# Optimization experiments

Measured on AMD Instinct MI355X. Metric: run time of the kernel, lower is better.

The kernel has to match this reference:

```python
import jax, jax.numpy as jnp
import numpy as np

B, N, L, D = 128, 1024, 512, 64


def setup_inputs() -> dict:
    key = jax.random.key(0)
    k1, k2 = jax.random.split(key)
    text_outputs = jax.random.normal(k1, (B, N, D), dtype=jnp.float32)
    image_outputs = jax.random.normal(k2, (B, L, D), dtype=jnp.float32)
    rng = np.random.RandomState(0)
    ntok = rng.randint(N // 4, N + 1, size=B)
    nreg = rng.randint(L // 4, L + 1, size=B)
    text_mask = (np.arange(N)[None, :] < ntok[:, None]).astype(np.float32)
    image_mask = (np.arange(L)[None, :] < nreg[:, None]).astype(np.float32)
    # impostor indices (torch code samples these with np.random inside forward;
    # here they are fixed constants for determinism), guaranteed != own index
    I_imp = rng.randint(0, B, size=B)
    S_imp = rng.randint(0, B, size=B)
    ar = np.arange(B)
    I_imp = np.where(I_imp == ar, (I_imp + 1) % B, I_imp).astype(np.int32)
    S_imp = np.where(S_imp == ar, (S_imp + 1) % B, S_imp).astype(np.int32)
    return {
        "text_outputs": text_outputs,
        "image_outputs": image_outputs,
        "text_mask": jnp.asarray(text_mask),
        "image_mask": jnp.asarray(image_mask),
        "I_imp_idx": jnp.asarray(I_imp),
        "S_imp_idx": jnp.asarray(S_imp),
    }


def _mean_max_sim(T, I, tmask, imask):
    # T: (N, D) tokens, I: (L, D) regions; masks select the ragged valid prefix.
    M = jnp.einsum('nd,ld->nl', T, I)                       # matchmap (N, L)
    neg = jnp.finfo(M.dtype).min
    mx = jnp.max(jnp.where(imask[None, :] > 0, M, neg), axis=1)  # max over regions
    return jnp.sum(mx * tmask) / jnp.sum(tmask)             # mean over valid tokens


def reference(text_outputs, image_outputs, text_mask, image_mask, I_imp_idx, S_imp_idx, margin=1.0):
    sim = jax.vmap(_mean_max_sim)
    anchor = sim(text_outputs, image_outputs, text_mask, image_mask)            # (B,)
    Simpsim = sim(text_outputs[S_imp_idx], image_outputs, text_mask[S_imp_idx], image_mask)
    Iimpsim = sim(text_outputs, image_outputs[I_imp_idx], text_mask, image_mask[I_imp_idx])
    # scalar per-sample hinge: term added only when margin+imp-anchor > 0 == relu
    per_sample = jax.nn.relu(margin + Iimpsim - anchor) + jax.nn.relu(margin + Simpsim - anchor)
    loss = jnp.sum(per_sample) / text_outputs.shape[0]
    return loss[None]  # torch returns shape (1,)
```

## Files before the change

kernel.cpp:

```cpp
#include <hip/hip_runtime.h>

#define B 128
#define N 1024
#define L 512
#define D 64

typedef float f32x4 __attribute__((ext_vector_type(4)));
typedef short bf16x8 __attribute__((ext_vector_type(8)));

__device__ inline unsigned int pack_bf16(float lo, float hi) {
    unsigned int a = __float_as_uint(lo), b = __float_as_uint(hi);
    a = (a + 0x7fffu + ((a >> 16) & 1u)) >> 16;
    b = (b + 0x7fffu + ((b >> 16) & 1u)) & 0xffff0000u;
    return a | b;
}

__global__ __launch_bounds__(256, 2) void sim_kernel(
        const float* __restrict__ T, const float* __restrict__ I,
        const float* __restrict__ tmask, const float* __restrict__ imask,
        const int* __restrict__ Iimp, const int* __restrict__ Simp,
        float* __restrict__ sims) {
    int blk = blockIdx.x;
    int s = blk >> 7;
    int b = blk & (B - 1);
    int Tb = b, Ib = b;
    if (s == 1) Tb = Simp[b];
    else if (s == 2) Ib = Iimp[b];

    int tid = threadIdx.x;
    int w = tid >> 6;
    int lane = tid & 63;
    int q = lane >> 4;
    int c = lane & 15;

    __shared__ unsigned short ldsI[L * D];
    float* redf = (float*)ldsI;

    float ts = 0.f, is = 0.f;
    {
        const float* tm = tmask + (size_t)Tb * N;
        for (int i = tid; i < N; i += 256) ts += tm[i];
        const float* im = imask + (size_t)Ib * L;
        for (int i = tid; i < L; i += 256) is += im[i];
    }
    for (int off = 32; off > 0; off >>= 1) {
        ts += __shfl_down(ts, off);
        is += __shfl_down(is, off);
    }
    if (lane == 0) { redf[w] = ts; redf[4 + w] = is; }
    __syncthreads();
    int ntok = (int)(redf[0] + redf[1] + redf[2] + redf[3] + 0.5f);
    int nreg = (int)(redf[4] + redf[5] + redf[6] + redf[7] + 0.5f);
    __syncthreads();

    int full_rt = nreg >> 4;
    int rem = nreg & 15;
    int nrt = full_rt + (rem ? 1 : 0);
    int nchunk = nrt * 128;
    const float* Ibase = I + (size_t)Ib * L * D;
    for (int ci = tid; ci < nchunk; ci += 256) {
        int rt = ci >> 7;
        int h = (ci >> 6) & 1;
        int ln = ci & 63;
        int r = rt * 16 + (ln & 15);
        int dbase = h * 32 + (ln >> 4) * 8;
        uint4 outv = make_uint4(0u, 0u, 0u, 0u);
        if (r < nreg) {
            const float4* p = (const float4*)(Ibase + (size_t)r * D + dbase);
            float4 f0 = p[0], f1 = p[1];
            outv.x = pack_bf16(f0.x, f0.y);
            outv.y = pack_bf16(f0.z, f0.w);
            outv.z = pack_bf16(f1.x, f1.y);
            outv.w = pack_bf16(f1.z, f1.w);
        }
        *(uint4*)((char*)ldsI + (size_t)ci * 16) = outv;
    }
    __syncthreads();

    const char* ldsB = (const char*)ldsI + (size_t)lane * 16;
    float bsum = 0.f;
    for (int tok0 = 0; tok0 < ntok; tok0 += 256) {
        int wt0 = tok0 + w * 64;
        bf16x8 afrag[4][2];
#pragma unroll
        for (int tt = 0; tt < 4; ++tt) {
            const float* trow = T + ((size_t)Tb * N + wt0 + tt * 16 + c) * D;
#pragma unroll
            for (int h = 0; h < 2; ++h) {
                const float4* p = (const float4*)(trow + h * 32 + q * 8);
                float4 f0 = p[0], f1 = p[1];
                unsigned int u[4];
                u[0] = pack_bf16(f0.x, f0.y);
                u[1] = pack_bf16(f0.z, f0.w);
                u[2] = pack_bf16(f1.x, f1.y);
                u[3] = pack_bf16(f1.z, f1.w);
                afrag[tt][h] = *(bf16x8*)u;
            }
        }

        float mx[4][4];
#pragma unroll
        for (int tt = 0; tt < 4; ++tt)
#pragma unroll
            for (int i = 0; i < 4; ++i) mx[tt][i] = -3.0e38f;

#pragma unroll 1
        for (int rt = 0; rt < full_rt; ++rt) {
            bf16x8 b0 = *(const bf16x8*)(ldsB + (size_t)(rt * 2 + 0) * 1024);
            bf16x8 b1 = *(const bf16x8*)(ldsB + (size_t)(rt * 2 + 1) * 1024);
#pragma unroll
            for (int tt = 0; tt < 4; ++tt) {
                f32x4 acc = {0.f, 0.f, 0.f, 0.f};
                acc = __builtin_amdgcn_mfma_f32_16x16x32_bf16(afrag[tt][0], b0, acc, 0, 0, 0);
                acc = __builtin_amdgcn_mfma_f32_16x16x32_bf16(afrag[tt][1], b1, acc, 0, 0, 0);
#pragma unroll
                for (int i = 0; i < 4; ++i) mx[tt][i] = fmaxf(mx[tt][i], acc[i]);
            }
        }
        if (rem) {
            bf16x8 b0 = *(const bf16x8*)(ldsB + (size_t)(full_rt * 2 + 0) * 1024);
            bf16x8 b1 = *(const bf16x8*)(ldsB + (size_t)(full_rt * 2 + 1) * 1024);
            bool valid = c < rem;
#pragma unroll
            for (int tt = 0; tt < 4; ++tt) {
                f32x4 acc = {0.f, 0.f, 0.f, 0.f};
                acc = __builtin_amdgcn_mfma_f32_16x16x32_bf16(afrag[tt][0], b0, acc, 0, 0, 0);
                acc = __builtin_amdgcn_mfma_f32_16x16x32_bf16(afrag[tt][1], b1, acc, 0, 0, 0);
                if (valid) {
#pragma unroll
                    for (int i = 0; i < 4; ++i) mx[tt][i] = fmaxf(mx[tt][i], acc[i]);
                }
            }
        }

#pragma unroll
        for (int m = 1; m < 16; m <<= 1) {
#pragma unroll
            for (int tt = 0; tt < 4; ++tt)
#pragma unroll
                for (int i = 0; i < 4; ++i)
                    mx[tt][i] = fmaxf(mx[tt][i], __shfl_xor(mx[tt][i], m));
        }
        if (c == 0) {
#pragma unroll
            for (int tt = 0; tt < 4; ++tt)
#pragma unroll
                for (int i = 0; i < 4; ++i) {
                    int row = wt0 + tt * 16 + q * 4 + i;
                    if (row < ntok) bsum += mx[tt][i];
                }
        }
    }

    for (int off = 32; off > 0; off >>= 1) bsum += __shfl_down(bsum, off);
    __syncthreads();
    if (lane == 0) redf[8 + w] = bsum;
    __syncthreads();
    if (tid == 0)
        sims[s * B + b] = (redf[8] + redf[9] + redf[10] + redf[11]) / (float)ntok;
}

__global__ void loss_kernel(const float* __restrict__ sims,
                            float* __restrict__ out) {
    int tid = threadIdx.x;
    float anc = sims[tid];
    float simp = sims[B + tid];
    float iimp = sims[2 * B + tid];
    float per = fmaxf(1.f + iimp - anc, 0.f) + fmaxf(1.f + simp - anc, 0.f);
    for (int off = 32; off > 0; off >>= 1) per += __shfl_down(per, off);
    __shared__ float w2[2];
    if ((tid & 63) == 0) w2[tid >> 6] = per;
    __syncthreads();
    if (tid == 0) out[0] = (w2[0] + w2[1]) / (float)B;
}

extern "C" void kernel_launch(void* const* d_in, const int* in_sizes, int n_in,
                              void* d_out, int out_size, void* d_ws, size_t ws_size,
                              hipStream_t stream) {
    const float* T     = (const float*)d_in[0];
    const float* I     = (const float*)d_in[1];
    const float* tmask = (const float*)d_in[2];
    const float* imask = (const float*)d_in[3];
    const int*   Iimp  = (const int*)d_in[4];
    const int*   Simp  = (const int*)d_in[5];
    float* sims = (float*)d_ws;

    sim_kernel<<<3 * B, 256, 0, stream>>>(T, I, tmask, imask, Iimp, Simp, sims);
    loss_kernel<<<1, 128, 0, stream>>>(sims, (float*)d_out);
}
```

Measured before the change: 138.4 us.

## Split token range across four blocks per pair and stream image tiles from global

```diff
diff --git a/kernel.cpp b/kernel.cpp
--- a/kernel.cpp
+++ b/kernel.cpp
@@ -1,4 +1,5 @@
 #include <hip/hip_runtime.h>
+#include <hip/hip_bf16.h>
 
 #define B 128
 #define N 1024
@@ -8,21 +9,25 @@
 typedef float f32x4 __attribute__((ext_vector_type(4)));
 typedef short bf16x8 __attribute__((ext_vector_type(8)));
 
-__device__ inline unsigned int pack_bf16(float lo, float hi) {
-    unsigned int a = __float_as_uint(lo), b = __float_as_uint(hi);
-    a = (a + 0x7fffu + ((a >> 16) & 1u)) >> 16;
-    b = (b + 0x7fffu + ((b >> 16) & 1u)) & 0xffff0000u;
-    return a | b;
+__device__ inline bf16x8 cvt8(float4 f0, float4 f1) {
+    union { __hip_bfloat162 h2[4]; bf16x8 v; } u;
+    u.h2[0] = __float22bfloat162_rn(make_float2(f0.x, f0.y));
+    u.h2[1] = __float22bfloat162_rn(make_float2(f0.z, f0.w));
+    u.h2[2] = __float22bfloat162_rn(make_float2(f1.x, f1.y));
+    u.h2[3] = __float22bfloat162_rn(make_float2(f1.z, f1.w));
+    return u.v;
 }
 
-__global__ __launch_bounds__(256, 2) void sim_kernel(
+__global__ __launch_bounds__(256, 4) void sim_kernel(
         const float* __restrict__ T, const float* __restrict__ I,
         const float* __restrict__ tmask, const float* __restrict__ imask,
         const int* __restrict__ Iimp, const int* __restrict__ Simp,
-        float* __restrict__ sims) {
+        float* __restrict__ partials) {
     int blk = blockIdx.x;
-    int s = blk >> 7;
-    int b = blk & (B - 1);
+    int chunk = blk & 3;
+    int bs = blk >> 2;
+    int b = bs & (B - 1);
+    int s = bs >> 7;
     int Tb = b, Ib = b;
     if (s == 1) Tb = Simp[b];
     else if (s == 2) Ib = Iimp[b];
@@ -33,8 +38,7 @@
     int q = lane >> 4;
     int c = lane & 15;
 
-    __shared__ unsigned short ldsI[L * D];
-    float* redf = (float*)ldsI;
+    __shared__ float red[12];
 
     float ts = 0.f, is = 0.f;
     {
@@ -47,131 +51,120 @@
         ts += __shfl_down(ts, off);
         is += __shfl_down(is, off);
     }
-    if (lane == 0) { redf[w] = ts; redf[4 + w] = is; }
+    if (lane == 0) { red[w] = ts; red[4 + w] = is; }
     __syncthreads();
-    int ntok = (int)(redf[0] + redf[1] + redf[2] + redf[3] + 0.5f);
-    int nreg = (int)(redf[4] + redf[5] + redf[6] + redf[7] + 0.5f);
-    __syncthreads();
+    int ntok = (int)(red[0] + red[1] + red[2] + red[3] + 0.5f);
+    int nreg = (int)(red[4] + red[5] + red[6] + red[7] + 0.5f);
+
+    int tok0 = chunk * 256;
+    if (tok0 >= ntok) {
+        if (tid == 0) partials[blk] = 0.f;
+        return;
+    }
+
+    int wt0 = tok0 + w * 64;
+    bf16x8 afrag[4][2];
+#pragma unroll
+    for (int tt = 0; tt < 4; ++tt) {
+        const float* trow = T + ((size_t)Tb * N + wt0 + tt * 16 + c) * D;
+#pragma unroll
+        for (int h = 0; h < 2; ++h) {
+            const float4* p = (const float4*)(trow + h * 32 + q * 8);
+            afrag[tt][h] = cvt8(p[0], p[1]);
+        }
+    }
+
+    float mx[4][4];
+#pragma unroll
+    for (int tt = 0; tt < 4; ++tt)
+#pragma unroll
+        for (int i = 0; i < 4; ++i) mx[tt][i] = -3.0e38f;
+
+    const float* Ip = I + (size_t)Ib * L * D + (size_t)c * D + q * 8;
 
     int full_rt = nreg >> 4;
     int rem = nreg & 15;
-    int nrt = full_rt + (rem ? 1 : 0);
-    int nchunk = nrt * 128;
-    const float* Ibase = I + (size_t)Ib * L * D;
-    for (int ci = tid; ci < nchunk; ci += 256) {
-        int rt = ci >> 7;
-        int h = (ci >> 6) & 1;
-        int ln = ci & 63;
-        int r = rt * 16 + (ln & 15);
-        int dbase = h * 32 + (ln >> 4) * 8;
-        uint4 outv = make_uint4(0u, 0u, 0u, 0u);
-        if (r < nreg) {
-            const float4* p = (const float4*)(Ibase + (size_t)r * D + dbase);
-            float4 f0 = p[0], f1 = p[1];
-            outv.x = pack_bf16(f0.x, f0.y);
-            outv.y = pack_bf16(f0.z, f0.w);
-            outv.z = pack_bf16(f1.x, f1.y);
-            outv.w = pack_bf16(f1.z, f1.w);
-        }
-        *(uint4*)((char*)ldsI + (size_t)ci * 16) = outv;
-    }
-    __syncthreads();
 
-    const char* ldsB = (const char*)ldsI + (size_t)lane * 16;
-    float bsum = 0.f;
-    for (int tok0 = 0; tok0 < ntok; tok0 += 256) {
-        int wt0 = tok0 + w * 64;
-        bf16x8 afrag[4][2];
+#pragma unroll 1
+    for (int rt = 0; rt < full_rt; ++rt) {
+        const float4* p0 = (const float4*)(Ip + (size_t)rt * 16 * D);
+        float4 f00 = p0[0], f01 = p0[1];
+        float4 f10 = p0[8], f11 = p0[9];
+        bf16x8 b0 = cvt8(f00, f01);
+        bf16x8 b1 = cvt8(f10, f11);
 #pragma unroll
         for (int tt = 0; tt < 4; ++tt) {
-            const float* trow = T + ((size_t)Tb * N + wt0 + tt * 16 + c) * D;
+            f32x4 acc = {0.f, 0.f, 0.f, 0.f};
+            acc = __builtin_amdgcn_mfma_f32_16x16x32_bf16(afrag[tt][0], b0, acc, 0, 0, 0);
+            acc = __builtin_amdgcn_mfma_f32_16x16x32_bf16(afrag[tt][1], b1, acc, 0, 0, 0);
 #pragma unroll
-            for (int h = 0; h < 2; ++h) {
-                const float4* p = (const float4*)(trow + h * 32 + q * 8);
-                float4 f0 = p[0], f1 = p[1];
-                unsigned int u[4];
-                u[0] = pack_bf16(f0.x, f0.y);
-                u[1] = pack_bf16(f0.z, f0.w);
-                u[2] = pack_bf16(f1.x, f1.y);
-                u[3] = pack_bf16(f1.z, f1.w);
-                afrag[tt][h] = *(bf16x8*)u;
-            }
+            for (int i = 0; i < 4; ++i) mx[tt][i] = fmaxf(mx[tt][i], acc[i]);
         }
-
-        float mx[4][4];
+    }
+    if (rem) {
+        const float4* p0 = (const float4*)(Ip + (size_t)full_rt * 16 * D);
+        bf16x8 b0 = cvt8(p0[0], p0[1]);
+        bf16x8 b1 = cvt8(p0[8], p0[9]);
+        bool valid = c < rem;
 #pragma unroll
-        for (int tt = 0; tt < 4; ++tt)
-#pragma unroll
-            for (int i = 0; i < 4; ++i) mx[tt][i] = -3.0e38f;
-
-#pragma unroll 1
-        for (int rt = 0; rt < full_rt; ++rt) {
-            bf16x8 b0 = *(const bf16x8*)(ldsB + (size_t)(rt * 2 + 0) * 1024);
-            bf16x8 b1 = *(const bf16x8*)(ldsB + (size_t)(rt * 2 + 1) * 1024);
-#pragma unroll
-            for (int tt = 0; tt < 4; ++tt) {
-                f32x4 acc = {0.f, 0.f, 0.f, 0.f};
-                acc = __builtin_amdgcn_mfma_f32_16x16x32_bf16(afrag[tt][0], b0, acc, 0, 0, 0);
-                acc = __builtin_amdgcn_mfma_f32_16x16x32_bf16(afrag[tt][1], b1, acc, 0, 0, 0);
+        for (int tt = 0; tt < 4; ++tt) {
+            f32x4 acc = {0.f, 0.f, 0.f, 0.f};
+            acc = __builtin_amdgcn_mfma_f32_16x16x32_bf16(afrag[tt][0], b0, acc, 0, 0, 0);
+            acc = __builtin_amdgcn_mfma_f32_16x16x32_bf16(afrag[tt][1], b1, acc, 0, 0, 0);
+            if (valid) {
 #pragma unroll
                 for (int i = 0; i < 4; ++i) mx[tt][i] = fmaxf(mx[tt][i], acc[i]);
             }
         }
-        if (rem) {
-            bf16x8 b0 = *(const bf16x8*)(ldsB + (size_t)(full_rt * 2 + 0) * 1024);
-            bf16x8 b1 = *(const bf16x8*)(ldsB + (size_t)(full_rt * 2 + 1) * 1024);
-            bool valid = c < rem;
-#pragma unroll
-            for (int tt = 0; tt < 4; ++tt) {
-                f32x4 acc = {0.f, 0.f, 0.f, 0.f};
-                acc = __builtin_amdgcn_mfma_f32_16x16x32_bf16(afrag[tt][0], b0, acc, 0, 0, 0);
-                acc = __builtin_amdgcn_mfma_f32_16x16x32_bf16(afrag[tt][1], b1, acc, 0, 0, 0);
-                if (valid) {
-#pragma unroll
-                    for (int i = 0; i < 4; ++i) mx[tt][i] = fmaxf(mx[tt][i], acc[i]);
-                }
-            }
-        }
+    }
 
 #pragma unroll
-        for (int m = 1; m < 16; m <<= 1) {
+    for (int m = 1; m < 16; m <<= 1) {
 #pragma unroll
-            for (int tt = 0; tt < 4; ++tt)
+        for (int tt = 0; tt < 4; ++tt)
 #pragma unroll
-                for (int i = 0; i < 4; ++i)
-                    mx[tt][i] = fmaxf(mx[tt][i], __shfl_xor(mx[tt][i], m));
-        }
-        if (c == 0) {
-#pragma unroll
-            for (int tt = 0; tt < 4; ++tt)
-#pragma unroll
-                for (int i = 0; i < 4; ++i) {
-                    int row = wt0 + tt * 16 + q * 4 + i;
-                    if (row < ntok) bsum += mx[tt][i];
-                }
-        }
+            for (int i = 0; i < 4; ++i)
+                mx[tt][i] = fmaxf(mx[tt][i], __shfl_xor(mx[tt][i], m));
     }
 
+    float bsum = 0.f;
+    if (c == 0) {
+#pragma unroll
+        for (int tt = 0; tt < 4; ++tt)
+#pragma unroll
+            for (int i = 0; i < 4; ++i) {
+                int row = wt0 + tt * 16 + q * 4 + i;
+                if (row < ntok) bsum += mx[tt][i];
+            }
+    }
     for (int off = 32; off > 0; off >>= 1) bsum += __shfl_down(bsum, off);
-    __syncthreads();
-    if (lane == 0) redf[8 + w] = bsum;
+    if (lane == 0) red[8 + w] = bsum;
     __syncthreads();
     if (tid == 0)
-        sims[s * B + b] = (redf[8] + redf[9] + redf[10] + redf[11]) / (float)ntok;
+        partials[blk] = (red[8] + red[9] + red[10] + red[11]) / (float)ntok;
 }
 
-__global__ void loss_kernel(const float* __restrict__ sims,
+__global__ void loss_kernel(const float* __restrict__ partials,
                             float* __restrict__ out) {
     int tid = threadIdx.x;
-    float anc = sims[tid];
-    float simp = sims[B + tid];
-    float iimp = sims[2 * B + tid];
-    float per = fmaxf(1.f + iimp - anc, 0.f) + fmaxf(1.f + simp - anc, 0.f);
+    __shared__ float simsL[384];
+    __shared__ float w6[6];
+    const float4* p4 = (const float4*)partials;
+    float4 v = p4[tid];
+    simsL[tid] = v.x + v.y + v.z + v.w;
+    __syncthreads();
+    float per = 0.f;
+    if (tid < B) {
+        float anc  = simsL[tid];
+        float simp = simsL[B + tid];
+        float iimp = simsL[2 * B + tid];
+        per = fmaxf(1.f + iimp - anc, 0.f) + fmaxf(1.f + simp - anc, 0.f);
+    }
     for (int off = 32; off > 0; off >>= 1) per += __shfl_down(per, off);
-    __shared__ float w2[2];
-    if ((tid & 63) == 0) w2[tid >> 6] = per;
+    if ((tid & 63) == 0) w6[tid >> 6] = per;
     __syncthreads();
-    if (tid == 0) out[0] = (w2[0] + w2[1]) / (float)B;
+    if (tid == 0)
+        out[0] = (w6[0] + w6[1] + w6[2] + w6[3] + w6[4] + w6[5]) / (float)B;
 }
 
 extern "C" void kernel_launch(void* const* d_in, const int* in_sizes, int n_in,
@@ -183,8 +176,8 @@
     const float* imask = (const float*)d_in[3];
     const int*   Iimp  = (const int*)d_in[4];
     const int*   Simp  = (const int*)d_in[5];
-    float* sims = (float*)d_ws;
+    float* partials = (float*)d_ws;
 
-    sim_kernel<<<3 * B, 256, 0, stream>>>(T, I, tmask, imask, Iimp, Simp, sims);
-    loss_kernel<<<1, 128, 0, stream>>>(sims, (float*)d_out);
+    sim_kernel<<<3 * B * 4, 256, 0, stream>>>(T, I, tmask, imask, Iimp, Simp, partials);
+    loss_kernel<<<1, 384, 0, stream>>>(partials, (float*)d_out);
 }
```

After: 183.1 us. 32.3% more time.
